# Kernel optimization log

Measured on AMD Instinct MI355X. Metric: run time of the kernel, lower is better.

## Reference

```python
import jax, jax.numpy as jnp
import numpy as np

N = 4096       # number of graph nodes
F_IN = 512     # in_features == out_features (residual connection requires it)
H = 8          # n_heads


def setup_inputs() -> dict:
    key = jax.random.key(0)
    k1, k2, k3, k4, k5 = jax.random.split(key, 5)
    s = 1.0 / np.sqrt(F_IN)  # keep projections well-scaled
    x = jax.random.normal(k1, (N, F_IN), dtype=jnp.float32)
    Wq = jax.random.normal(k2, (F_IN, F_IN), dtype=jnp.float32) * s
    Wk = jax.random.normal(k3, (F_IN, F_IN), dtype=jnp.float32) * s
    Wv = jax.random.normal(k4, (F_IN, F_IN), dtype=jnp.float32) * s
    adj = jax.random.randint(k5, (H, N, N), 0, 2, dtype=jnp.int32)
    return {"x": x, "Wq": Wq, "Wk": Wk, "Wv": Wv, "adj": adj}


def reference(x, Wq, Wk, Wv, adj):
    # Faithful to torch GraphAttentionLayer.forward (eval mode, dropout off).
    # NOTE: the torch code builds keys = input.repeat(N,1,1).detach() -> the
    # K/V inputs are stop-gradient copies of x; projections are per-node, so
    # we compute them once instead of materializing the redundant [N,N,F].
    n, f = x.shape
    d = f // H  # head dim (chunk_size)
    xk = jax.lax.stop_gradient(x)
    # nn.Linear: y = x @ W.T ; split feature dim into heads -> [H, N, d]
    Q = (x @ Wq.T).reshape(n, H, d).transpose(1, 0, 2)
    K = (xk @ Wk.T).reshape(n, H, d).transpose(1, 0, 2)
    V = (xk @ Wv.T).reshape(n, H, d).transpose(1, 0, 2)
    # scaled by sqrt(in_features) (NOT head dim), as in the original
    scores = jnp.einsum('hnd,hmd->hnm', Q, K) / jnp.sqrt(jnp.float32(f))
    scores = jnp.where(adj > 0, scores, jnp.float32(-9e15))
    attn = jax.nn.softmax(scores, axis=-1)          # [H, N, N]
    out = jnp.einsum('hnm,hmd->hnd', attn, V)       # [H, N, d]
    out = out.transpose(1, 0, 2).reshape(n, f)      # concat heads -> [N, F]
    return jax.nn.elu(out + x)[:, None, :]          # [N, 1, F] like torch
```

## Files before the change

### kernel.cpp

```cpp
#include <hip/hip_runtime.h>
#include <hip/hip_bf16.h>

#define NN 4096
#define FF 512
#define NH 8
#define DH 64

typedef __attribute__((ext_vector_type(8))) short bf16x8;
typedef __attribute__((ext_vector_type(4))) float f32x4;

#define X_OFF  0
#define W_OFF  2097152
#define QF_OFF 2883584
#define KF_OFF 4980736
#define VF_OFF 7077888
#define PACC_OFF 9175040
#define PDEN_USHORT_OFF 17563648

__device__ __forceinline__ ushort f2bf(float f) {
    __hip_bfloat16 h = __float2bfloat16(f);
    return __builtin_bit_cast(ushort, h);
}
__device__ __forceinline__ float bf2f(ushort u) {
    unsigned int v = ((unsigned int)u) << 16;
    return __builtin_bit_cast(float, v);
}

__global__ __launch_bounds__(256) void cvt_kernel(const float* __restrict__ x,
                                                  const float* __restrict__ wq,
                                                  const float* __restrict__ wk,
                                                  const float* __restrict__ wv,
                                                  ushort* __restrict__ ws) {
    int i = blockIdx.x * 256 + threadIdx.x;
    int base = i * 4;
    const float* src;
    int off;
    float sc = 1.f;
    if (base < 2097152) { src = x; off = base; }
    else {
        int t = base - 2097152;
        int m = t >> 18;
        src = (m == 0) ? wq : ((m == 1) ? wk : wv);
        if (m == 0) sc = 0.044194173824159216f;
        off = t & 262143;
    }
    float4 v = *reinterpret_cast<const float4*>(src + off);
    ushort4 o;
    o.x = f2bf(v.x * sc); o.y = f2bf(v.y * sc); o.z = f2bf(v.z * sc); o.w = f2bf(v.w * sc);
    *reinterpret_cast<ushort4*>(ws + base) = o;
}

__global__ __launch_bounds__(256) void qkv_kernel(ushort* __restrict__ ws) {
    int bx = blockIdx.x;
    int mat = bx >> 3;
    int fb  = bx & 7;
    int mb  = blockIdx.y;
    int wave = threadIdx.x >> 6, lane = threadIdx.x & 63;
    int la = lane & 15, lk = lane >> 4;

    int m_base = mb * 64 + wave * 16;
    int f_base = fb * 64;

    const ushort* xb = ws + X_OFF;
    const ushort* wb = ws + W_OFF + mat * 262144;

    f32x4 acc[4];
#pragma unroll
    for (int t = 0; t < 4; ++t) acc[t] = (f32x4){0.f, 0.f, 0.f, 0.f};

#pragma unroll 4
    for (int k0 = 0; k0 < 512; k0 += 32) {
        bf16x8 a = *reinterpret_cast<const bf16x8*>(xb + (size_t)(m_base + la) * 512 + k0 + lk * 8);
#pragma unroll
        for (int ft = 0; ft < 4; ++ft) {
            bf16x8 b = *reinterpret_cast<const bf16x8*>(wb + (size_t)(f_base + ft * 16 + la) * 512 + k0 + lk * 8);
            acc[ft] = __builtin_amdgcn_mfma_f32_16x16x32_bf16(a, b, acc[ft], 0, 0, 0);
        }
    }

#pragma unroll
    for (int ft = 0; ft < 4; ++ft) {
#pragma unroll
        for (int r = 0; r < 4; ++r) {
            int n = m_base + lk * 4 + r;
            int d = ft * 16 + la;
            ushort v = f2bf(acc[ft][r]);
            if (mat < 2) {
                ushort* base = ws + (mat == 0 ? QF_OFF : KF_OFF) + (size_t)fb * 262144;
                int blk = n >> 4, rr = n & 15;
                int half = d >> 5, lkk = (d >> 3) & 3, e = d & 7;
                base[(((size_t)blk * 2 + half) * 64 + lkk * 16 + rr) * 8 + e] = v;
            } else {
                ushort* base = ws + VF_OFF + (size_t)fb * 262144;
                int kb64 = n >> 6, kc = n & 63;
                int hf = kc >> 5, lkv = (kc >> 3) & 3, ev = kc & 7;
                int dt = d >> 4, lav = d & 15;
                base[((((size_t)kb64 * 4 + dt) * 2 + hf) * 64 + lkv * 16 + lav) * 8 + ev] = v;
            }
        }
    }
}


#define STAGE(BUF, KB)                                                                     \
    {                                                                                      \
        const ushort* sbase_ = (wave < 2) ? Kh : Vh;                                       \
        ushort(*dbuf_)[512] = (wave < 2) ? kbuf[BUF] : vbuf[BUF];                          \
        int t0_ = (wave & 1) * 4;                                                          \
        _Pragma("unroll")                                                                  \
        for (int t_ = 0; t_ < 4; ++t_) {                                                   \
            int tile_ = t0_ + t_;                                                          \
            const ushort* src_ = sbase_ +                                                  \
                (((size_t)(KB) * 4 + (tile_ >> 1)) * 2 + (tile_ & 1)) * 512 + lane * 8;    \
            __builtin_amdgcn_global_load_lds(                                              \
                (const __attribute__((address_space(1))) unsigned int*)src_,               \
                (__attribute__((address_space(3))) unsigned int*)&dbuf_[tile_][0],         \
                16, 0, 0);                                                                 \
        }                                                                                  \
    }

__global__ __launch_bounds__(256, 3) void attn_kernel(const int* __restrict__ adj,
                                                      const ushort* __restrict__ ws,
                                                      ushort* __restrict__ pacc,
                                                      float* __restrict__ pden) {
    __shared__ ushort kbuf[2][8][512];
    __shared__ ushort vbuf[2][8][512];
    __shared__ ushort P[4][16][72];

    int bid = blockIdx.x;
    int h = bid & 7, qb = (bid >> 3) & 63, ks = bid >> 9;
    int wave = threadIdx.x >> 6, lane = threadIdx.x & 63;
    int la = lane & 15, lk = lane >> 4;
    int q0w = qb * 64 + wave * 16;

    const ushort* Qh = ws + QF_OFF + (size_t)h * 262144;
    const ushort* Kh = ws + KF_OFF + (size_t)h * 262144;
    const ushort* Vh = ws + VF_OFF + (size_t)h * 262144;
    const int* adjw = adj + (size_t)h * 16777216 + (size_t)q0w * 4096;

    bf16x8 qa0 = *reinterpret_cast<const bf16x8*>(Qh + ((((size_t)(q0w >> 4)) * 2 + 0) * 64 + lane) * 8);
    bf16x8 qa1 = *reinterpret_cast<const bf16x8*>(Qh + ((((size_t)(q0w >> 4)) * 2 + 1) * 64 + lane) * 8);

    f32x4 acc[4];
    float den[4];
#pragma unroll
    for (int r = 0; r < 4; ++r) {
        acc[r] = (f32x4){0.f, 0.f, 0.f, 0.f};
        den[r] = 0.f;
    }

    const f32x4 zero = {0.f, 0.f, 0.f, 0.f};
    int kbase = ks * 16;

    STAGE(0, kbase)
    int adjv[16];
#pragma unroll
    for (int kt = 0; kt < 4; ++kt)
#pragma unroll
        for (int r = 0; r < 4; ++r)
            adjv[kt * 4 + r] = __builtin_nontemporal_load(
                adjw + (size_t)(lk * 4 + r) * 4096 + (size_t)kbase * 64 + kt * 16 + la);
    __syncthreads();

    for (int it = 0; it < 16; ++it) {
        int kb = kbase + it;
        int cur = it & 1;

        if (it < 15) STAGE(cur ^ 1, kb + 1)

        float fmask[16];
#pragma unroll
        for (int j = 0; j < 16; ++j)
            fmask[j] = adjv[j] ? 0.f : -1e30f;

        if (it < 15) {
#pragma unroll
            for (int kt = 0; kt < 4; ++kt)
#pragma unroll
                for (int r = 0; r < 4; ++r)
                    adjv[kt * 4 + r] = __builtin_nontemporal_load(
                        adjw + (size_t)(lk * 4 + r) * 4096 + (size_t)(kb + 1) * 64 + kt * 16 + la);
        }

        f32x4 s[4];
#pragma unroll
        for (int kt = 0; kt < 4; ++kt) {
            bf16x8 kf0 = *reinterpret_cast<const bf16x8*>(&kbuf[cur][kt * 2 + 0][lane * 8]);
            bf16x8 kf1 = *reinterpret_cast<const bf16x8*>(&kbuf[cur][kt * 2 + 1][lane * 8]);
            s[kt] = __builtin_amdgcn_mfma_f32_16x16x32_bf16(qa0, kf0, zero, 0, 0, 0);
            s[kt] = __builtin_amdgcn_mfma_f32_16x16x32_bf16(qa1, kf1, s[kt], 0, 0, 0);
        }

#pragma unroll
        for (int kt = 0; kt < 4; ++kt)
#pragma unroll
            for (int r = 0; r < 4; ++r) {
                float e = __expf(s[kt][r] + fmask[kt * 4 + r]);
                den[r] += e;
                P[wave][lk * 4 + r][kt * 16 + la] = f2bf(e);
            }

        bf16x8 pa0 = *reinterpret_cast<const bf16x8*>(&P[wave][la][lk * 8]);
        bf16x8 pa1 = *reinterpret_cast<const bf16x8*>(&P[wave][la][32 + lk * 8]);
#pragma unroll
        for (int dt = 0; dt < 4; ++dt) {
            bf16x8 vb0 = *reinterpret_cast<const bf16x8*>(&vbuf[cur][dt * 2 + 0][lane * 8]);
            bf16x8 vb1 = *reinterpret_cast<const bf16x8*>(&vbuf[cur][dt * 2 + 1][lane * 8]);
            acc[dt] = __builtin_amdgcn_mfma_f32_16x16x32_bf16(pa0, vb0, acc[dt], 0, 0, 0);
            acc[dt] = __builtin_amdgcn_mfma_f32_16x16x32_bf16(pa1, vb1, acc[dt], 0, 0, 0);
        }

        __syncthreads();
    }

#pragma unroll
    for (int r = 0; r < 4; ++r)
#pragma unroll
        for (int mm = 1; mm < 16; mm <<= 1)
            den[r] += __shfl_xor(den[r], mm, 64);

    ushort* pa_out = pacc + ((size_t)ks * 8 + h) * 4096 * 64;
#pragma unroll
    for (int dt = 0; dt < 4; ++dt)
#pragma unroll
        for (int r = 0; r < 4; ++r) {
            int q = q0w + lk * 4 + r;
            __builtin_nontemporal_store(f2bf(acc[dt][r]), pa_out + (size_t)q * 64 + dt * 16 + la);
        }
    if (la == 0) {
        float* pd = pden + ((size_t)ks * 8 + h) * 4096;
#pragma unroll
        for (int r = 0; r < 4; ++r)
            pd[q0w + lk * 4 + r] = den[r];
    }
}

__global__ __launch_bounds__(256) void combine_kernel(const float* __restrict__ x,
                                                      const ushort* __restrict__ pacc,
                                                      const float* __restrict__ pden,
                                                      float* __restrict__ out) {
    int idx = blockIdx.x * 256 + threadIdx.x;
    int n = idx >> 7, fq = idx & 127;
    int h = fq >> 4;
    int d4 = (fq & 15) * 4;

    float4 o = make_float4(0.f, 0.f, 0.f, 0.f);
    float den = 0.f;
#pragma unroll
    for (int ksp = 0; ksp < 4; ++ksp) {
        const ushort* pa = pacc + (((size_t)ksp * 8 + h) * 4096 + n) * 64 + d4;
        ushort4 p = *reinterpret_cast<const ushort4*>(pa);
        o.x += bf2f(p.x); o.y += bf2f(p.y); o.z += bf2f(p.z); o.w += bf2f(p.w);
        den += pden[((size_t)ksp * 8 + h) * 4096 + n];
    }
    float4 xv = *reinterpret_cast<const float4*>(x + (size_t)n * 512 + fq * 4);
    float inv = 1.f / den;
    float4 r;
    r.x = o.x * inv + xv.x;
    r.y = o.y * inv + xv.y;
    r.z = o.z * inv + xv.z;
    r.w = o.w * inv + xv.w;
    r.x = (r.x > 0.f) ? r.x : (__expf(r.x) - 1.f);
    r.y = (r.y > 0.f) ? r.y : (__expf(r.y) - 1.f);
    r.z = (r.z > 0.f) ? r.z : (__expf(r.z) - 1.f);
    r.w = (r.w > 0.f) ? r.w : (__expf(r.w) - 1.f);
    *reinterpret_cast<float4*>(out + (size_t)n * 512 + fq * 4) = r;
}

extern "C" void kernel_launch(void* const* d_in, const int* in_sizes, int n_in,
                              void* d_out, int out_size, void* d_ws, size_t ws_size,
                              hipStream_t stream) {
    const float* x  = (const float*)d_in[0];
    const float* wq = (const float*)d_in[1];
    const float* wk = (const float*)d_in[2];
    const float* wv = (const float*)d_in[3];
    const int*   adj = (const int*)d_in[4];
    float* out = (float*)d_out;
    ushort* ws = (ushort*)d_ws;
    ushort* pacc = ws + PACC_OFF;
    float* pden = (float*)(ws + PDEN_USHORT_OFF);

    cvt_kernel<<<2816, 256, 0, stream>>>(x, wq, wk, wv, ws);
    qkv_kernel<<<dim3(24, 64), 256, 0, stream>>>(ws);
    attn_kernel<<<2048, 256, 0, stream>>>(adj, ws, pacc, pden);
    combine_kernel<<<2048, 256, 0, stream>>>(x, pacc, pden, out);
}
```

Baseline: 222.7 us.

## Unroll attention loop by two with two-deep adjacency prefetch and explicit vmcnt waits

The key-block loop is rewritten as a macro body unrolled twice. The adjacency mask now alternates between two register sets, so it is prefetched two iterations ahead instead of one. The trailing __syncthreads is replaced by an explicit s_waitcnt vmcnt(16) plus s_barrier at the start of each iteration, so only the K/V tile and mask for the current step must have landed. sched_barrier fences keep the compiler from reordering the issue of mask loads and LDS staging. The goal is to hide the large adj read latency better, at the cost of extra registers and a fragile hand-counted vmcnt.

```diff
diff --git a/kernel.cpp b/kernel.cpp
--- a/kernel.cpp
+++ b/kernel.cpp
@@ -119,6 +119,53 @@
         }                                                                                  \
     }
 
+#define BODY(ADJ, KB, DOSTAGE, SKB, DOADJ, AKB, VM)                                        \
+    {                                                                                      \
+        asm volatile("s_waitcnt vmcnt(" #VM ")" ::: "memory");                             \
+        __builtin_amdgcn_s_barrier();                                                      \
+        const int cur_ = (KB) & 1;                                                         \
+        float fmask[16];                                                                   \
+        _Pragma("unroll")                                                                  \
+        for (int j = 0; j < 16; ++j) fmask[j] = ADJ[j] ? 0.f : -1e30f;                     \
+        __builtin_amdgcn_sched_barrier(0);                                                 \
+        if (DOSTAGE) STAGE(((KB) + 1) & 1, SKB)                                            \
+        __builtin_amdgcn_sched_barrier(0);                                                 \
+        if (DOADJ) {                                                                       \
+            _Pragma("unroll")                                                              \
+            for (int kt = 0; kt < 4; ++kt)                                                 \
+                _Pragma("unroll")                                                          \
+                for (int r = 0; r < 4; ++r)                                                \
+                    ADJ[kt * 4 + r] = __builtin_nontemporal_load(                          \
+                        adjw + (size_t)(lk * 4 + r) * 4096 + (size_t)(AKB) * 64 + kt * 16 + la); \
+        }                                                                                  \
+        __builtin_amdgcn_sched_barrier(0);                                                 \
+        f32x4 s[4];                                                                        \
+        _Pragma("unroll")                                                                  \
+        for (int kt = 0; kt < 4; ++kt) {                                                   \
+            bf16x8 kf0 = *reinterpret_cast<const bf16x8*>(&kbuf[cur_][kt * 2 + 0][lane * 8]); \
+            bf16x8 kf1 = *reinterpret_cast<const bf16x8*>(&kbuf[cur_][kt * 2 + 1][lane * 8]); \
+            s[kt] = __builtin_amdgcn_mfma_f32_16x16x32_bf16(qa0, kf0, zero, 0, 0, 0);      \
+            s[kt] = __builtin_amdgcn_mfma_f32_16x16x32_bf16(qa1, kf1, s[kt], 0, 0, 0);     \
+        }                                                                                  \
+        _Pragma("unroll")                                                                  \
+        for (int kt = 0; kt < 4; ++kt)                                                     \
+            _Pragma("unroll")                                                              \
+            for (int r = 0; r < 4; ++r) {                                                  \
+                float e = __expf(s[kt][r] + fmask[kt * 4 + r]);                            \
+                den[r] += e;                                                               \
+                P[wave][lk * 4 + r][kt * 16 + la] = f2bf(e);                               \
+            }                                                                              \
+        bf16x8 pa0 = *reinterpret_cast<const bf16x8*>(&P[wave][la][lk * 8]);               \
+        bf16x8 pa1 = *reinterpret_cast<const bf16x8*>(&P[wave][la][32 + lk * 8]);          \
+        _Pragma("unroll")                                                                  \
+        for (int dt = 0; dt < 4; ++dt) {                                                   \
+            bf16x8 vb0 = *reinterpret_cast<const bf16x8*>(&vbuf[cur_][dt * 2 + 0][lane * 8]); \
+            bf16x8 vb1 = *reinterpret_cast<const bf16x8*>(&vbuf[cur_][dt * 2 + 1][lane * 8]); \
+            acc[dt] = __builtin_amdgcn_mfma_f32_16x16x32_bf16(pa0, vb0, acc[dt], 0, 0, 0); \
+            acc[dt] = __builtin_amdgcn_mfma_f32_16x16x32_bf16(pa1, vb1, acc[dt], 0, 0, 0); \
+        }                                                                                  \
+    }
+
 __global__ __launch_bounds__(256, 3) void attn_kernel(const int* __restrict__ adj,
                                                       const ushort* __restrict__ ws,
                                                       ushort* __restrict__ pacc,
@@ -152,66 +199,31 @@
     const f32x4 zero = {0.f, 0.f, 0.f, 0.f};
     int kbase = ks * 16;
 
+    int adjA[16], adjB[16];
+#pragma unroll
+    for (int kt = 0; kt < 4; ++kt)
+#pragma unroll
+        for (int r = 0; r < 4; ++r)
+            adjA[kt * 4 + r] = __builtin_nontemporal_load(
+                adjw + (size_t)(lk * 4 + r) * 4096 + (size_t)kbase * 64 + kt * 16 + la);
+    __builtin_amdgcn_sched_barrier(0);
     STAGE(0, kbase)
-    int adjv[16];
+    __builtin_amdgcn_sched_barrier(0);
 #pragma unroll
     for (int kt = 0; kt < 4; ++kt)
 #pragma unroll
         for (int r = 0; r < 4; ++r)
-            adjv[kt * 4 + r] = __builtin_nontemporal_load(
-                adjw + (size_t)(lk * 4 + r) * 4096 + (size_t)kbase * 64 + kt * 16 + la);
-    __syncthreads();
-
-    for (int it = 0; it < 16; ++it) {
-        int kb = kbase + it;
-        int cur = it & 1;
-
-        if (it < 15) STAGE(cur ^ 1, kb + 1)
-
-        float fmask[16];
-#pragma unroll
-        for (int j = 0; j < 16; ++j)
-            fmask[j] = adjv[j] ? 0.f : -1e30f;
-
-        if (it < 15) {
-#pragma unroll
-            for (int kt = 0; kt < 4; ++kt)
-#pragma unroll
-                for (int r = 0; r < 4; ++r)
-                    adjv[kt * 4 + r] = __builtin_nontemporal_load(
-                        adjw + (size_t)(lk * 4 + r) * 4096 + (size_t)(kb + 1) * 64 + kt * 16 + la);
-        }
-
-        f32x4 s[4];
-#pragma unroll
-        for (int kt = 0; kt < 4; ++kt) {
-            bf16x8 kf0 = *reinterpret_cast<const bf16x8*>(&kbuf[cur][kt * 2 + 0][lane * 8]);
-            bf16x8 kf1 = *reinterpret_cast<const bf16x8*>(&kbuf[cur][kt * 2 + 1][lane * 8]);
-            s[kt] = __builtin_amdgcn_mfma_f32_16x16x32_bf16(qa0, kf0, zero, 0, 0, 0);
-            s[kt] = __builtin_amdgcn_mfma_f32_16x16x32_bf16(qa1, kf1, s[kt], 0, 0, 0);
-        }
-
-#pragma unroll
-        for (int kt = 0; kt < 4; ++kt)
-#pragma unroll
-            for (int r = 0; r < 4; ++r) {
-                float e = __expf(s[kt][r] + fmask[kt * 4 + r]);
-                den[r] += e;
-                P[wave][lk * 4 + r][kt * 16 + la] = f2bf(e);
-            }
-
-        bf16x8 pa0 = *reinterpret_cast<const bf16x8*>(&P[wave][la][lk * 8]);
-        bf16x8 pa1 = *reinterpret_cast<const bf16x8*>(&P[wave][la][32 + lk * 8]);
-#pragma unroll
-        for (int dt = 0; dt < 4; ++dt) {
-            bf16x8 vb0 = *reinterpret_cast<const bf16x8*>(&vbuf[cur][dt * 2 + 0][lane * 8]);
-            bf16x8 vb1 = *reinterpret_cast<const bf16x8*>(&vbuf[cur][dt * 2 + 1][lane * 8]);
-            acc[dt] = __builtin_amdgcn_mfma_f32_16x16x32_bf16(pa0, vb0, acc[dt], 0, 0, 0);
-            acc[dt] = __builtin_amdgcn_mfma_f32_16x16x32_bf16(pa1, vb1, acc[dt], 0, 0, 0);
-        }
-
-        __syncthreads();
-    }
+            adjB[kt * 4 + r] = __builtin_nontemporal_load(
+                adjw + (size_t)(lk * 4 + r) * 4096 + (size_t)(kbase + 1) * 64 + kt * 16 + la);
+    __builtin_amdgcn_sched_barrier(0);
+
+    for (int it = 0; it < 14; it += 2) {
+        int kbA = kbase + it;
+        BODY(adjA, kbA,     1, kbA + 1, 1, kbA + 2, 16)
+        BODY(adjB, kbA + 1, 1, kbA + 2, 1, kbA + 3, 16)
+    }
+    BODY(adjA, kbase + 14, 1, kbase + 15, 0, 0, 16)
+    BODY(adjB, kbase + 15, 0, 0,          0, 0, 0)
 
 #pragma unroll
     for (int r = 0; r < 4; ++r)
```

Result: faster. 210.6 us (-5.4%).
